# Performance work log

Hardware: AMD Instinct MI355X
Metric: run time of the kernel (lower is better)

The kernel has to match this reference:

```python
import jax, jax.numpy as jnp
import numpy as np


def setup_inputs() -> dict:
    key = jax.random.key(0)
    k1, k2, k3, k4 = jax.random.split(key, 4)
    n_nodes, n_edges, d_in, d_half = 100000, 1600000, 256, 128
    x = jax.random.normal(k1, (n_nodes, d_in), dtype=jnp.float32)
    edge_index = jax.random.randint(k2, (2, n_edges), 0, n_nodes, dtype=jnp.int64)
    W_f = jax.random.normal(k3, (d_half, d_in), dtype=jnp.float32) * (1.0 / np.sqrt(d_in))
    W_b = jax.random.normal(k4, (d_half, d_in), dtype=jnp.float32) * (1.0 / np.sqrt(d_in))
    bias_param = jnp.zeros((2 * d_half,), dtype=jnp.float32)
    return {"x": x, "edge_index": edge_index, "W_f": W_f, "W_b": W_b, "bias_param": bias_param}


def _inv_sqrt(deg):
    # deg.pow(-0.5) with inf -> 0
    return jnp.where(deg > 0, jax.lax.rsqrt(deg), 0.0)


def reference(x, edge_index, W_f, W_b, bias_param):
    n_nodes = x.shape[0]
    # add_remaining_self_loops with fill value 1
    loops = jnp.arange(n_nodes, dtype=edge_index.dtype)
    ei = jnp.concatenate([edge_index, jnp.stack([loops, loops])], axis=1)
    n_e = ei.shape[1]
    w = jnp.ones((n_e,), dtype=x.dtype)
    # directed_norm, flow='source_to_target': col, row = edge_index
    col, row = ei[0], ei[1]
    in_deg = jax.ops.segment_sum(w, col, num_segments=n_nodes)
    out_deg = jax.ops.segment_sum(w, row, num_segments=n_nodes)
    ew = _inv_sqrt(out_deg)[row] * w * _inv_sqrt(in_deg)[col]  # [E]
    # adj_forward: source=row, target=col ; adj_backward: source=col, target=row
    mf = (x @ W_f.T)[row] * ew[:, None]           # [E, d_half]
    y_forward = jax.ops.segment_sum(mf, col, num_segments=n_nodes)
    mb = (x @ W_b.T)[col] * ew[:, None]           # [E, d_half]
    y_backward = jax.ops.segment_sum(mb, row, num_segments=n_nodes)
    y = jnp.concatenate([y_forward, y_backward], axis=-1) + bias_param
    return y
```

## Files before the change

### kernel.cpp

```cpp
#include <hip/hip_runtime.h>

#define D_IN 256
#define D_HALF 128

typedef __attribute__((ext_vector_type(8))) short short8;
typedef __attribute__((ext_vector_type(4))) float float4v;

__device__ __forceinline__ unsigned short f2bf(float f) {
    union { float f; unsigned u; } v; v.f = f;
    unsigned r = v.u + 0x7FFF + ((v.u >> 16) & 1);
    return (unsigned short)(r >> 16);
}
__device__ __forceinline__ float bflo(unsigned u) { union { unsigned u; float f; } v; v.u = u << 16; return v.f; }
__device__ __forceinline__ float bfhi(unsigned u) { union { unsigned u; float f; } v; v.u = u & 0xffff0000u; return v.f; }

__device__ __forceinline__ void async16(const void* g, void* l) {
    __builtin_amdgcn_global_load_lds(
        (const __attribute__((address_space(1))) unsigned int*)g,
        (__attribute__((address_space(3))) unsigned int*)l, 16, 0, 0);
}


#define S_SH 9
#define NBK_MAX 512
#define CAP 12288
#define EPB 4096

__global__ void zero_kernel(int* __restrict__ gcnt) {
    int i = blockIdx.x * blockDim.x + threadIdx.x;
    if (i < NBK_MAX) gcnt[i] = 0;
}

__global__ void p1_kernel(const int* __restrict__ col, const int* __restrict__ row,
                          int* __restrict__ gcnt, unsigned* __restrict__ staging,
                          int N, int E) {
    __shared__ int hist[NBK_MAX];
    __shared__ int base_[NBK_MAX];
    const int tid = threadIdx.x;
    hist[tid] = 0; hist[tid + 256] = 0;
    __syncthreads();

    int ce[16], re[16];
    const int e0 = blockIdx.x * EPB;
    #pragma unroll
    for (int j = 0; j < 16; ++j) {
        int e = e0 + j * 256 + tid;
        if (e < E) {
            ce[j] = col[e];
            re[j] = row[e];
            atomicAdd(&hist[ce[j] >> S_SH], 1);
            atomicAdd(&hist[(N + re[j]) >> S_SH], 1);
        } else {
            ce[j] = -1; re[j] = 0;
        }
    }
    __syncthreads();

    #pragma unroll
    for (int b = 0; b < NBK_MAX / 256; ++b) {
        int idx = b * 256 + tid;
        int c = hist[idx];
        if (c) base_[idx] = idx * CAP + atomicAdd(&gcnt[idx], c);
    }
    __syncthreads();
    hist[tid] = 0; hist[tid + 256] = 0;
    __syncthreads();

    #pragma unroll
    for (int j = 0; j < 16; ++j) {
        if (ce[j] >= 0) {
            int c = ce[j], r = re[j];
            int bf = c >> S_SH;
            int rf = atomicAdd(&hist[bf], 1);
            staging[(size_t)base_[bf] + rf] = ((unsigned)(c & 511) << 23) | (unsigned)r;
            int sb = N + r;
            int bb = sb >> S_SH;
            int rb = atomicAdd(&hist[bb], 1);
            staging[(size_t)base_[bb] + rb] = ((unsigned)(sb & 511) << 23) | (unsigned)c;
        }
    }
}

__global__ void scanB_kernel(const int* __restrict__ gcnt, int* __restrict__ bbase, int nbuck) {
    __shared__ int s[NBK_MAX];
    const int tid = threadIdx.x;
    int v = (tid < nbuck) ? gcnt[tid] : 0;
    s[tid] = v;
    __syncthreads();
    for (int d = 1; d < NBK_MAX; d <<= 1) {
        int t = (tid >= d) ? s[tid - d] : 0;
        __syncthreads();
        s[tid] += t;
        __syncthreads();
    }
    if (tid < nbuck) bbase[tid] = s[tid] - v;
}

__global__ void bsort_kernel(const unsigned* __restrict__ staging, const int* __restrict__ gcnt,
                             const int* __restrict__ bbase, int* __restrict__ cnt,
                             int* __restrict__ offs, int* __restrict__ adj, int M) {
    __shared__ int lcnt[NBK_MAX];
    __shared__ int s[256];
    __shared__ int lbuf[CAP];
    const int tid = threadIdx.x;
    const int b = blockIdx.x;
    const int s0 = b << S_SH;
    lcnt[tid] = 0; lcnt[tid + 256] = 0;
    __syncthreads();

    const int count = gcnt[b];
    const int base = bbase[b];
    const unsigned* __restrict__ st = staging + (size_t)b * CAP;

    for (int i = tid; i < count; i += 256)
        atomicAdd(&lcnt[st[i] >> 23], 1);
    __syncthreads();

    int v0 = lcnt[2 * tid], v1 = lcnt[2 * tid + 1];
    int pair = v0 + v1;
    s[tid] = pair;
    __syncthreads();
    for (int d = 1; d < 256; d <<= 1) {
        int t = (tid >= d) ? s[tid - d] : 0;
        __syncthreads();
        s[tid] += t;
        __syncthreads();
    }
    int excl = s[tid] - pair;

    int gs0 = s0 + 2 * tid;
    if (gs0 < M)     { cnt[gs0] = v0;     offs[gs0] = base + excl; }
    if (gs0 + 1 < M) { cnt[gs0 + 1] = v1; offs[gs0 + 1] = base + excl + v0; }

    lcnt[2 * tid] = excl;
    lcnt[2 * tid + 1] = excl + v0;
    __syncthreads();

    for (int i = tid; i < count; i += 256) {
        unsigned it = st[i];
        int sl = it >> 23;
        int p = atomicAdd(&lcnt[sl], 1);
        lbuf[p] = (int)(it & 0x7fffffu);
    }
    __syncthreads();
    for (int i = tid; i < count; i += 256)
        adj[base + i] = lbuf[i];
}

__global__ void inv_kernel(const int* __restrict__ cnt,
                           float* __restrict__ inv_in, float* __restrict__ inv_out, int N) {
    int i = blockIdx.x * blockDim.x + threadIdx.x;
    if (i < N) {
        inv_in[i]  = rsqrtf((float)(cnt[i] + 1));
        inv_out[i] = rsqrtf((float)(cnt[N + i] + 1));
    }
}


__global__ void cast_kernel(const float* __restrict__ x, const float* __restrict__ Wf,
                            const float* __restrict__ Wb, unsigned short* __restrict__ xb,
                            unsigned short* __restrict__ wcat, int n4) {
    int i = blockIdx.x * blockDim.x + threadIdx.x;
    const int w4 = (2 * D_HALF * D_IN) / 4;
    if (i < n4) {
        float4 v = ((const float4*)x)[i];
        ushort4 o = { f2bf(v.x), f2bf(v.y), f2bf(v.z), f2bf(v.w) };
        ((ushort4*)xb)[i] = o;
    } else if (i < n4 + w4) {
        int j = i - n4;
        int elem = j * 4;
        const float* src = (elem < D_HALF * D_IN) ? (Wf + elem) : (Wb + (elem - D_HALF * D_IN));
        float4 v = *(const float4*)src;
        ushort4 o = { f2bf(v.x), f2bf(v.y), f2bf(v.z), f2bf(v.w) };
        ((ushort4*)wcat)[j] = o;
    }
}


#define BM 128
#define BN 128
#define BK 32

__global__ void gemm_mfma_kernel(const unsigned short* __restrict__ xb,
                                 const unsigned short* __restrict__ wcat,
                                 const float* __restrict__ inv_in,
                                 const float* __restrict__ inv_out,
                                 unsigned short* __restrict__ zb, int N) {
    __shared__ __align__(16) unsigned short As[BM * BK];
    __shared__ __align__(16) unsigned short Bs[BN * BK];
    const int tid = threadIdx.x;
    const int wave = tid >> 6;
    const int lane = tid & 63;
    const int bm = blockIdx.x * BM;
    const int bn = blockIdx.y * BN;
    const int warpM = wave >> 1;
    const int warpN = wave & 1;
    const int l15 = lane & 15;
    const int quad = lane >> 4;

    float4v acc[4][4];
    #pragma unroll
    for (int i = 0; i < 4; ++i)
        #pragma unroll
        for (int j = 0; j < 4; ++j)
            acc[i][j] = (float4v){0.f, 0.f, 0.f, 0.f};

    for (int kt = 0; kt < D_IN / BK; ++kt) {
        #pragma unroll
        for (int iss = 0; iss < 2; ++iss) {
            const int pbase = iss * 256 + wave * 64;
            const int p = pbase + lane;
            const int m = p >> 2;
            const int g = (p & 3) ^ ((m >> 1) & 3);
            int gm = bm + m; if (gm >= N) gm = N - 1;
            async16(xb + (size_t)gm * D_IN + kt * BK + g * 8, &As[pbase * 8]);
            async16(wcat + (size_t)(bn + m) * D_IN + kt * BK + g * 8, &Bs[pbase * 8]);
        }
        __syncthreads();

        short8 af[4], bfr[4];
        #pragma unroll
        for (int mi = 0; mi < 4; ++mi) {
            int m = warpM * 64 + mi * 16 + l15;
            af[mi] = *(const short8*)&As[m * BK + (quad ^ ((m >> 1) & 3)) * 8];
        }
        #pragma unroll
        for (int ni = 0; ni < 4; ++ni) {
            int n = warpN * 64 + ni * 16 + l15;
            bfr[ni] = *(const short8*)&Bs[n * BK + (quad ^ ((n >> 1) & 3)) * 8];
        }
        #pragma unroll
        for (int mi = 0; mi < 4; ++mi)
            #pragma unroll
            for (int ni = 0; ni < 4; ++ni)
                acc[mi][ni] = __builtin_amdgcn_mfma_f32_16x16x32_bf16(af[mi], bfr[ni], acc[mi][ni], 0, 0, 0);
        __syncthreads();
    }

    const float* __restrict__ sc = (blockIdx.y == 0) ? inv_out : inv_in;
    #pragma unroll
    for (int mi = 0; mi < 4; ++mi) {
        #pragma unroll
        for (int reg = 0; reg < 4; ++reg) {
            int gm = bm + warpM * 64 + mi * 16 + quad * 4 + reg;
            if (gm < N) {
                float s = sc[gm];
                #pragma unroll
                for (int ni = 0; ni < 4; ++ni) {
                    int gn = bn + warpN * 64 + ni * 16 + l15;
                    zb[(size_t)gm * D_IN + gn] = f2bf(acc[mi][ni][reg] * s);
                }
            }
        }
    }
}


__global__ void gather_kernel(const unsigned short* __restrict__ zb, const int* __restrict__ adj,
                              const int* __restrict__ offs, const int* __restrict__ cnt,
                              const float* __restrict__ inv_in, const float* __restrict__ inv_out,
                              const float* __restrict__ bias,
                              float* __restrict__ out, int N) {
    const int wave = threadIdx.x >> 6;
    const int lane = threadIdx.x & 63;
    const int slot = blockIdx.x * 4 + wave;
    if (slot >= 2 * N) return;
    const int node = slot >> 1;
    const int dir = slot & 1;
    const int csr = dir * N + node;
    const int beg = offs[csr];
    const int deg = cnt[csr];
    const int end = beg + deg;
    const int choff = dir * D_HALF + 2 * lane;

    float a0 = 0.f, a1 = 0.f, b0 = 0.f, b1 = 0.f;
    for (int base = beg; base < end; base += 64) {
        int len = end - base; if (len > 64) len = 64;
        int nb = (lane < len) ? adj[base + lane] : node;
        for (int j0 = 0; j0 < len; j0 += 8) {
            #pragma unroll
            for (int jj = 0; jj < 8; ++jj) {
                const int j = j0 + jj;
                float m = (j < len) ? 1.0f : 0.0f;
                int n0 = __builtin_amdgcn_readlane(nb, j);
                unsigned u0 = *(const unsigned*)&zb[(size_t)n0 * D_IN + choff];
                if (jj & 1) {
                    b0 = fmaf(m, bflo(u0), b0);
                    b1 = fmaf(m, bfhi(u0), b1);
                } else {
                    a0 = fmaf(m, bflo(u0), a0);
                    a1 = fmaf(m, bfhi(u0), a1);
                }
            }
        }
    }
    unsigned us = *(const unsigned*)&zb[(size_t)node * D_IN + choff];
    a0 += b0 + bflo(us);
    a1 += b1 + bfhi(us);

    const float scale = dir ? inv_out[node] : inv_in[node];
    size_t oi = (size_t)node * D_IN + choff;
    float2 o;
    o.x = bias[choff]     + scale * a0;
    o.y = bias[choff + 1] + scale * a1;
    *(float2*)&out[oi] = o;
}


extern "C" void kernel_launch(void* const* d_in, const int* in_sizes, int n_in,
                              void* d_out, int out_size, void* d_ws, size_t ws_size,
                              hipStream_t stream) {
    const float* x    = (const float*)d_in[0];
    const int*   ei   = (const int*)d_in[1];
    const float* Wf   = (const float*)d_in[2];
    const float* Wb   = (const float*)d_in[3];
    const float* bias = (const float*)d_in[4];
    float* out = (float*)d_out;

    const int N = in_sizes[0] / D_IN;
    const int E = in_sizes[1] / 2;
    const int* col = ei;
    const int* rowp = ei + E;

    char* ws = (char*)d_ws;
    unsigned short* xb = (unsigned short*)ws;   ws += (size_t)N * D_IN * sizeof(short);
    unsigned short* zb = (unsigned short*)ws;   ws += (size_t)N * D_IN * sizeof(short);
    unsigned short* wcat = (unsigned short*)ws; ws += (size_t)2 * D_HALF * D_IN * sizeof(short);
    int* cnt = (int*)ws;            ws += (size_t)2 * N * sizeof(int);
    int* offs = (int*)ws;           ws += (size_t)2 * N * sizeof(int);
    float* inv_in = (float*)ws;     ws += (size_t)N * sizeof(float);
    float* inv_out = (float*)ws;    ws += (size_t)N * sizeof(float);
    int* adj = (int*)ws;            ws += (size_t)2 * E * sizeof(int);
    int* gcnt = (int*)ws;           ws += NBK_MAX * sizeof(int);
    int* bbase = (int*)ws;          ws += NBK_MAX * sizeof(int);

    unsigned* staging = (unsigned*)zb;

    const int M = 2 * N;
    const int nbuck = (M + 511) >> S_SH;

    const int n4 = N * D_IN / 4;
    const int w4 = (2 * D_HALF * D_IN) / 4;
    cast_kernel<<<(n4 + w4 + 255) / 256, 256, 0, stream>>>(x, Wf, Wb, xb, wcat, n4);

    zero_kernel<<<2, 256, 0, stream>>>(gcnt);
    p1_kernel<<<(E + EPB - 1) / EPB, 256, 0, stream>>>(col, rowp, gcnt, staging, N, E);
    scanB_kernel<<<1, NBK_MAX, 0, stream>>>(gcnt, bbase, nbuck);
    bsort_kernel<<<nbuck, 256, 0, stream>>>(staging, gcnt, bbase, cnt, offs, adj, M);
    inv_kernel<<<(N + 255) / 256, 256, 0, stream>>>(cnt, inv_in, inv_out, N);

    dim3 ggrid((N + BM - 1) / BM, D_IN / BN);
    gemm_mfma_kernel<<<ggrid, 256, 0, stream>>>(xb, wcat, inv_in, inv_out, zb, N);

    gather_kernel<<<(2 * N + 3) / 4, 256, 0, stream>>>(zb, adj, offs, cnt, inv_in, inv_out, bias, out, N);
}
```

Baseline: 395.7 us.

## Gather four neighbors per wave step with 16-byte loads and cross-group reduction

Restructures the gather kernel so each wave is split into four 16-lane groups. Each group handles a different neighbor per step and each lane loads 16 bytes (8 bf16 channels) instead of 4 bytes. Partial sums are combined with xor shuffles at the end. This cuts the serialized per-neighbor loop iterations and uses wider memory transactions, at the cost of more accumulator registers, a reduction step, and masked wasted lanes for low-degree nodes.

```diff
diff --git a/kernel.cpp b/kernel.cpp
--- a/kernel.cpp
+++ b/kernel.cpp
@@ -271,39 +271,56 @@
     const int beg = offs[csr];
     const int deg = cnt[csr];
     const int end = beg + deg;
-    const int choff = dir * D_HALF + 2 * lane;
-
-    float a0 = 0.f, a1 = 0.f, b0 = 0.f, b1 = 0.f;
+    const int g4 = lane >> 4;
+    const int l15 = lane & 15;
+    const int chu = dir * D_HALF + 8 * l15;
+    const int pa = g4 << 2;
+
+    float a0 = 0.f, a1 = 0.f, a2 = 0.f, a3 = 0.f;
+    float a4 = 0.f, a5 = 0.f, a6 = 0.f, a7 = 0.f;
+
     for (int base = beg; base < end; base += 64) {
         int len = end - base; if (len > 64) len = 64;
         int nb = (lane < len) ? adj[base + lane] : node;
-        for (int j0 = 0; j0 < len; j0 += 8) {
-            #pragma unroll
-            for (int jj = 0; jj < 8; ++jj) {
-                const int j = j0 + jj;
-                float m = (j < len) ? 1.0f : 0.0f;
-                int n0 = __builtin_amdgcn_readlane(nb, j);
-                unsigned u0 = *(const unsigned*)&zb[(size_t)n0 * D_IN + choff];
-                if (jj & 1) {
-                    b0 = fmaf(m, bflo(u0), b0);
-                    b1 = fmaf(m, bfhi(u0), b1);
-                } else {
-                    a0 = fmaf(m, bflo(u0), a0);
-                    a1 = fmaf(m, bfhi(u0), a1);
-                }
-            }
-        }
-    }
-    unsigned us = *(const unsigned*)&zb[(size_t)node * D_IN + choff];
-    a0 += b0 + bflo(us);
-    a1 += b1 + bfhi(us);
-
-    const float scale = dir ? inv_out[node] : inv_in[node];
-    size_t oi = (size_t)node * D_IN + choff;
-    float2 o;
-    o.x = bias[choff]     + scale * a0;
-    o.y = bias[choff + 1] + scale * a1;
-    *(float2*)&out[oi] = o;
+        #pragma unroll 8
+        for (int j0 = 0; j0 < len; j0 += 4) {
+            int nsel = __builtin_amdgcn_ds_bpermute((j0 << 2) + pa, nb);
+            float m = (j0 + g4 < len) ? 1.0f : 0.0f;
+            const uint4 u = *(const uint4*)&zb[(size_t)nsel * D_IN + chu];
+            a0 = fmaf(m, bflo(u.x), a0); a1 = fmaf(m, bfhi(u.x), a1);
+            a2 = fmaf(m, bflo(u.y), a2); a3 = fmaf(m, bfhi(u.y), a3);
+            a4 = fmaf(m, bflo(u.z), a4); a5 = fmaf(m, bfhi(u.z), a5);
+            a6 = fmaf(m, bflo(u.w), a6); a7 = fmaf(m, bfhi(u.w), a7);
+        }
+    }
+
+    a0 += __shfl_xor(a0, 16); a0 += __shfl_xor(a0, 32);
+    a1 += __shfl_xor(a1, 16); a1 += __shfl_xor(a1, 32);
+    a2 += __shfl_xor(a2, 16); a2 += __shfl_xor(a2, 32);
+    a3 += __shfl_xor(a3, 16); a3 += __shfl_xor(a3, 32);
+    a4 += __shfl_xor(a4, 16); a4 += __shfl_xor(a4, 32);
+    a5 += __shfl_xor(a5, 16); a5 += __shfl_xor(a5, 32);
+    a6 += __shfl_xor(a6, 16); a6 += __shfl_xor(a6, 32);
+    a7 += __shfl_xor(a7, 16); a7 += __shfl_xor(a7, 32);
+
+    if (g4 == 0) {
+        const uint4 us = *(const uint4*)&zb[(size_t)node * D_IN + chu];
+        a0 += bflo(us.x); a1 += bfhi(us.x);
+        a2 += bflo(us.y); a3 += bfhi(us.y);
+        a4 += bflo(us.z); a5 += bfhi(us.z);
+        a6 += bflo(us.w); a7 += bfhi(us.w);
+
+        const float scale = dir ? inv_out[node] : inv_in[node];
+        const float4 bv0 = *(const float4*)&bias[chu];
+        const float4 bv1 = *(const float4*)&bias[chu + 4];
+        size_t oi = (size_t)node * D_IN + chu;
+        float4 o0 = { bv0.x + scale * a0, bv0.y + scale * a1,
+                      bv0.z + scale * a2, bv0.w + scale * a3 };
+        float4 o1 = { bv1.x + scale * a4, bv1.y + scale * a5,
+                      bv1.z + scale * a6, bv1.w + scale * a7 };
+        *(float4*)&out[oi] = o0;
+        *(float4*)&out[oi + 4] = o1;
+    }
 }
 
 
```

Result: no change. 400.8 us (+1.3%).
